# Optimization experiments

Hardware: AMD Instinct MI355X
Metric: run time of the kernel (lower is better)

## Reference

```python
import jax, jax.numpy as jnp
import numpy as np

B, S, G, F, L = 8192, 1152, 576, 16, 24  # batch, n_sites, n_symm, features, lattice side
NP = 576  # number of plaquette correlators (= L^2)


def log_cosh(t):
    # numerically stable log(cosh(t)) as in netket.nn.log_cosh
    a = jnp.abs(t)
    return a + jnp.log1p(jnp.exp(-2.0 * a)) - jnp.log(2.0)


def setup_inputs() -> dict:
    key = jax.random.key(0)
    k = jax.random.split(key, 22)
    p = lambda kk, shape: 0.01 * jax.random.normal(kk, shape, jnp.float32)
    inp = {
        "x": jax.random.normal(k[0], (B, S), jnp.float32),
        "hidden_bias": p(k[1], (F,)),
        "symm_kernel": p(k[2], (F, S)),
        "visible_bias": p(k[3], (2,)),
        "corr0_bias": p(k[4], (1,)),
        "corr0_kernel": p(k[5], (F, NP)),
        "corr1_bias": p(k[6], (1,)),
        "corr1_kernel": p(k[7], (F, L)),
        "corr2_bias": p(k[8], (1,)),
        "corr2_kernel": p(k[9], (F, L)),
        "loop0_hidden_bias": p(k[10], (F,)),
        "loop0_kernel": p(k[11], (F, L)),
        "loop1_hidden_bias": p(k[12], (F,)),
        "loop1_kernel": p(k[13], (F, L)),
        "symmetries": jax.random.randint(k[14], (G, S), 0, S, jnp.int32),
        "corr0_idx": jax.random.randint(k[15], (NP, 4), 0, S, jnp.int32),
        "corr0_symm": jax.random.randint(k[16], (G, NP), 0, NP, jnp.int32),
        "corr1_idx": jax.random.randint(k[17], (L, L), 0, S, jnp.int32),
        "corr1_symm": jax.random.randint(k[18], (G, L), 0, L, jnp.int32),
        "corr2_idx": jax.random.randint(k[19], (L, L), 0, S, jnp.int32),
        "corr2_symm": jax.random.randint(k[20], (G, L), 0, L, jnp.int32),
    }
    return inp


def reference(x, hidden_bias, symm_kernel, visible_bias,
              corr0_bias, corr0_kernel, corr1_bias, corr1_kernel,
              corr2_bias, corr2_kernel,
              loop0_hidden_bias, loop0_kernel, loop1_hidden_bias, loop1_kernel,
              symmetries, corr0_idx, corr0_symm, corr1_idx, corr1_symm,
              corr2_idx, corr2_symm):
    # symmetrized single-spin term: (B, F, G)
    theta = jnp.einsum('bs,fgs->bfg', x, symm_kernel[:, symmetries])
    theta = theta + hidden_bias[None, :, None]
    # sublattice visible bias: (B,)
    bias = jnp.sum(x.reshape(x.shape[0], -1, 2), axis=1) @ visible_bias

    corr_vals = []
    for idx, sidx, cb, ck in ((corr0_idx, corr0_symm, corr0_bias, corr0_kernel),
                              (corr1_idx, corr1_symm, corr1_bias, corr1_kernel),
                              (corr2_idx, corr2_symm, corr2_bias, corr2_kernel)):
        cv = jnp.take(x, idx, axis=1).prod(axis=2)  # (B, n_corr)
        corr_vals.append(cv)
        theta = theta + jnp.einsum('bc,fgc->bfg', cv, ck[:, sidx])
        bias = bias + cb[0] * jnp.sum(cv, axis=1)

    out = jnp.sum(log_cosh(theta), axis=(1, 2)) + bias

    # extra hidden units for the last two (loop) correlators
    for cv, sidx, lhb, lk in ((corr_vals[1], corr1_symm, loop0_hidden_bias, loop0_kernel),
                              (corr_vals[2], corr2_symm, loop1_hidden_bias, loop1_kernel)):
        lt = jnp.einsum('bc,fgc->bfg', cv, lk[:, sidx]) + lhb[None, :, None]
        out = out + jnp.sum(log_cosh(lt), axis=(1, 2))
    return out
```

## Files before the change

### kernel.cpp

```cpp
#include <hip/hip_runtime.h>
#include <hip/hip_bf16.h>

#define B_   8192
#define S_   1152
#define G_   576
#define F_   16
#define L_   24
#define NP_  576
#define KA   1856
#define NCOL 9216
#define KV   1984

typedef float f32x4 __attribute__((ext_vector_type(4)));
typedef short short8_t __attribute__((ext_vector_type(8)));

__device__ __forceinline__ short f2bf(float v) {
  unsigned u = __float_as_uint(v);
  unsigned r = (u + 0x7fffu + ((u >> 16) & 1u)) >> 16;
  return (short)r;
}
__device__ __forceinline__ float bf2f(short s) {
  return __uint_as_float(((unsigned)(unsigned short)s) << 16);
}

__device__ __forceinline__ float log_cosh_f(float t) {
  float a = fabsf(t);
  return a + __logf(1.f + __expf(-2.f * a)) - 0.6931471805599453f;
}

__device__ __forceinline__ float wave_sum(float v) {
  #pragma unroll
  for (int d = 1; d < 64; d <<= 1) v += __shfl_xor(v, d, 64);
  return v;
}

__device__ __forceinline__ void load_lds16(const void* g, void* l) {
  __builtin_amdgcn_global_load_lds(
      (const __attribute__((address_space(1))) void*)g,
      (__attribute__((address_space(3))) void*)l, 16, 0, 0);
}

__global__ __launch_bounds__(256) void build_a_kernel(
    const float* __restrict__ x, const float* __restrict__ vb,
    const float* __restrict__ cb0, const float* __restrict__ cb1,
    const float* __restrict__ cb2,
    const int* __restrict__ idx0, const int* __restrict__ idx1,
    const int* __restrict__ idx2,
    short* __restrict__ A, float* __restrict__ out) {
  int b = blockIdx.x, t = threadIdx.x;
  __shared__ float xs[S_];
  __shared__ float red[20];
  float se = 0.f, so = 0.f, s0 = 0.f, s1 = 0.f, s2 = 0.f;
  const float* xr = x + (size_t)b * S_;
  short* Ar = A + (size_t)b * KA;

  for (int i = t; i < S_; i += 256) {
    float v = xr[i];
    xs[i] = v;
    Ar[i] = f2bf(v);
    if (i & 1) so += v; else se += v;
  }
  __syncthreads();

  for (int c = t; c < NP_; c += 256) {
    const int* q = idx0 + c * 4;
    float p = xs[q[0]] * xs[q[1]] * xs[q[2]] * xs[q[3]];
    s0 += p;
    Ar[S_ + c] = f2bf(p);
  }
  if (t < L_) {
    const int* q = idx1 + t * L_;
    float p = 1.f;
    #pragma unroll
    for (int j = 0; j < L_; ++j) p *= xs[q[j]];
    s1 = p;
    short hi = f2bf(p);
    Ar[1728 + t] = hi;
    Ar[1752 + t] = f2bf(p - bf2f(hi));
  }
  if (t >= 32 && t < 32 + L_) {
    int l = t - 32;
    const int* q = idx2 + l * L_;
    float p = 1.f;
    #pragma unroll
    for (int j = 0; j < L_; ++j) p *= xs[q[j]];
    s2 = p;
    short hi = f2bf(p);
    Ar[1792 + l] = hi;
    Ar[1816 + l] = f2bf(p - bf2f(hi));
  }
  if (t >= 64 && t < 80) Ar[1776 + (t - 64)] = 0;
  if (t >= 80 && t < 96) Ar[1840 + (t - 80)] = 0;

  se = wave_sum(se); so = wave_sum(so);
  s0 = wave_sum(s0); s1 = wave_sum(s1); s2 = wave_sum(s2);
  int w = t >> 6;
  if ((t & 63) == 0) {
    red[w] = se; red[4 + w] = so; red[8 + w] = s0;
    red[12 + w] = s1; red[16 + w] = s2;
  }
  __syncthreads();
  if (t == 0) {
    float a  = red[0] + red[1] + red[2] + red[3];
    float bb = red[4] + red[5] + red[6] + red[7];
    float c0 = red[8] + red[9] + red[10] + red[11];
    float c1 = red[12] + red[13] + red[14] + red[15];
    float c2 = red[16] + red[17] + red[18] + red[19];
    out[b] = vb[0] * a + vb[1] * bb + cb0[0] * c0 + cb1[0] * c1 + cb2[0] * c2;
  }
}

__global__ __launch_bounds__(256) void build_w_kernel(
    const float* __restrict__ symm_kernel, const int* __restrict__ symmetries,
    const float* __restrict__ c0k, const int* __restrict__ c0s,
    const float* __restrict__ c1k, const int* __restrict__ c1s,
    const float* __restrict__ c2k, const int* __restrict__ c2s,
    const float* __restrict__ l0k, const float* __restrict__ l1k,
    short* __restrict__ Wt, short* __restrict__ Wlt) {
  const int CHUNKS = KV / 8;
  int t = blockIdx.x * 256 + threadIdx.x;
  int n = t / CHUNKS;
  if (n >= NCOL) return;
  int ch = t - n * CHUNKS;
  int g = n >> 4, f = n & 15;
  int k0 = ch * 8;
  short8_t pack;
  #pragma unroll
  for (int j = 0; j < 8; ++j) {
    int k = k0 + j;
    float val;
    if (k < 1152) {
      val = symm_kernel[f * S_ + symmetries[g * S_ + k]];
    } else if (k < 1728) {
      int c = k - 1152;
      val = c0k[f * NP_ + c0s[g * NP_ + c]];
    } else if (k < 1792) {
      int c = k - 1728;
      val = (c < 48) ? c1k[f * L_ + c1s[g * L_ + (c < 24 ? c : c - 24)]] : 0.f;
    } else if (k < 1856) {
      int c = k - 1792;
      val = (c < 48) ? c2k[f * L_ + c2s[g * L_ + (c < 24 ? c : c - 24)]] : 0.f;
    } else if (k < 1920) {
      int c = k - 1856;
      val = (c < 48) ? l0k[f * L_ + c1s[g * L_ + (c < 24 ? c : c - 24)]] : 0.f;
    } else {
      int c = k - 1920;
      val = (c < 48) ? l1k[f * L_ + c2s[g * L_ + (c < 24 ? c : c - 24)]] : 0.f;
    }
    pack[j] = f2bf(val);
  }
  if (k0 < KA) *(short8_t*)(Wt + (size_t)n * KA + k0) = pack;
  else         *(short8_t*)(Wlt + (size_t)n * 128 + (k0 - KA)) = pack;
}

__global__ __launch_bounds__(256) void gemm_fused(
    const short* __restrict__ A, const short* __restrict__ Wt,
    const short* __restrict__ Wlt,
    const float* __restrict__ hidden_bias, const float* __restrict__ l0hb,
    const float* __restrict__ l1hb, float* __restrict__ out) {
  __shared__ short Als[3][128 * 64];
  __shared__ short Bls[3][128 * 64];
  const int tid = threadIdx.x;
  const int w = tid >> 6, lane = tid & 63;
  const int wm = w >> 1, wn = w & 1;
  const int lr = lane & 15, lg = lane >> 4;

  const int bid = blockIdx.x;
  const int xcd = bid & 7;
  const int idx = bid >> 3;
  const int st  = idx >> 6;
  const int u   = idx & 63;
  const int m0 = (xcd * 8 + (u & 7)) * 128;
  const int n0 = (st * 8 + (u >> 3)) * 128;

  const int srow = tid >> 3;
  const int scol = ((tid & 7) ^ (srow & 7)) * 16;

  f32x4 acc[4][4];
  float rs[4][4];
  #pragma unroll
  for (int i = 0; i < 4; ++i)
    #pragma unroll
    for (int j = 0; j < 4; ++j) {
      #pragma unroll
      for (int q = 0; q < 4; ++q) acc[i][j][q] = 0.f;
      rs[i][j] = 0.f;
    }

  const char* Abase = (const char*)A + (size_t)m0 * (KA * 2);
  const char* Wbase = (const char*)Wt + (size_t)n0 * (KA * 2);
  const char* Lbase = (const char*)Wlt + (size_t)n0 * 256;

  auto stage = [&](int buf, size_t aOff, const char* bSrc, size_t bStride, size_t bOff) {
    #pragma unroll
    for (int i = 0; i < 4; ++i) {
      int row = i * 32 + srow;
      load_lds16(Abase + (size_t)row * (KA * 2) + aOff + scol,
                 (char*)&Als[buf][0] + (i * 256 + w * 64) * 16);
      load_lds16(bSrc + (size_t)row * bStride + bOff + scol,
                 (char*)&Bls[buf][0] + (i * 256 + w * 64) * 16);
    }
  };

  auto compute = [&](int buf) {
    #pragma unroll
    for (int kk = 0; kk < 2; ++kk) {
      short8_t af[4], wf[4];
      #pragma unroll
      for (int mi = 0; mi < 4; ++mi) {
        int row = wm * 64 + mi * 16 + lr;
        af[mi] = *(const short8_t*)&Als[buf][row * 64 + (((kk * 4 + lg) ^ (lr & 7)) * 8)];
      }
      #pragma unroll
      for (int ni = 0; ni < 4; ++ni) {
        int row = wn * 64 + ni * 16 + lr;
        wf[ni] = *(const short8_t*)&Bls[buf][row * 64 + (((kk * 4 + lg) ^ (lr & 7)) * 8)];
      }
      #pragma unroll
      for (int mi = 0; mi < 4; ++mi)
        #pragma unroll
        for (int ni = 0; ni < 4; ++ni)
          acc[mi][ni] = __builtin_amdgcn_mfma_f32_16x16x32_bf16(af[mi], wf[ni], acc[mi][ni], 0, 0, 0);
    }
  };

  const size_t WS = (size_t)(KA * 2);

  stage(0, 0, Wbase, WS, 0);
  stage(1, 128, Wbase, WS, 128);

  int bc = 0;
  for (int t = 0; t < 29; ++t) {
    if (t + 2 <= 28) {
      int bs = bc + 2; if (bs >= 3) bs -= 3;
      stage(bs, (size_t)(t + 2) * 128, Wbase, WS, (size_t)(t + 2) * 128);
    }
    __builtin_amdgcn_sched_barrier(0);
    if (t < 27)       asm volatile("s_waitcnt vmcnt(16)" ::: "memory");
    else if (t == 27) asm volatile("s_waitcnt vmcnt(8)" ::: "memory");
    else              asm volatile("s_waitcnt vmcnt(0)" ::: "memory");
    __builtin_amdgcn_sched_barrier(0);
    __builtin_amdgcn_s_barrier();
    __builtin_amdgcn_sched_barrier(0);
    compute(bc);
    __builtin_amdgcn_sched_barrier(0);
    __builtin_amdgcn_s_barrier();
    __builtin_amdgcn_sched_barrier(0);
    bc = bc + 1; if (bc >= 3) bc = 0;
  }

  stage(0, (size_t)1728 * 2, Lbase, 256, 0);
  stage(1, (size_t)1792 * 2, Lbase, 256, 128);

  {
    float hb = hidden_bias[lr];
    #pragma unroll
    for (int mi = 0; mi < 4; ++mi)
      #pragma unroll
      for (int i = 0; i < 4; ++i) {
        float s = 0.f;
        #pragma unroll
        for (int ni = 0; ni < 4; ++ni) s += log_cosh_f(acc[mi][ni][i] + hb);
        rs[mi][i] += s;
      }
  }
  __syncthreads();

  #pragma unroll
  for (int pass = 0; pass < 2; ++pass) {
    #pragma unroll
    for (int i = 0; i < 4; ++i)
      #pragma unroll
      for (int j = 0; j < 4; ++j)
        #pragma unroll
        for (int q = 0; q < 4; ++q) acc[i][j][q] = 0.f;

    compute(pass);

    float lb = (pass == 0 ? l0hb : l1hb)[lr];
    #pragma unroll
    for (int mi = 0; mi < 4; ++mi)
      #pragma unroll
      for (int i = 0; i < 4; ++i) {
        float s = 0.f;
        #pragma unroll
        for (int ni = 0; ni < 4; ++ni) s += log_cosh_f(acc[mi][ni][i] + lb);
        rs[mi][i] += s;
      }
  }

  #pragma unroll
  for (int mi = 0; mi < 4; ++mi)
    #pragma unroll
    for (int i = 0; i < 4; ++i) {
      float v = rs[mi][i];
      v += __shfl_xor(v, 1, 64);
      v += __shfl_xor(v, 2, 64);
      v += __shfl_xor(v, 4, 64);
      v += __shfl_xor(v, 8, 64);
      if (lr == 0) atomicAdd(&out[m0 + wm * 64 + mi * 16 + lg * 4 + i], v);
    }
}

extern "C" void kernel_launch(void* const* d_in, const int* in_sizes, int n_in,
                              void* d_out, int out_size, void* d_ws, size_t ws_size,
                              hipStream_t stream) {
  const float* x            = (const float*)d_in[0];
  const float* hidden_bias  = (const float*)d_in[1];
  const float* symm_kernel  = (const float*)d_in[2];
  const float* visible_bias = (const float*)d_in[3];
  const float* corr0_bias   = (const float*)d_in[4];
  const float* corr0_kernel = (const float*)d_in[5];
  const float* corr1_bias   = (const float*)d_in[6];
  const float* corr1_kernel = (const float*)d_in[7];
  const float* corr2_bias   = (const float*)d_in[8];
  const float* corr2_kernel = (const float*)d_in[9];
  const float* l0hb         = (const float*)d_in[10];
  const float* l0k          = (const float*)d_in[11];
  const float* l1hb         = (const float*)d_in[12];
  const float* l1k          = (const float*)d_in[13];
  const int* symmetries     = (const int*)d_in[14];
  const int* idx0           = (const int*)d_in[15];
  const int* c0s            = (const int*)d_in[16];
  const int* idx1           = (const int*)d_in[17];
  const int* c1s            = (const int*)d_in[18];
  const int* idx2           = (const int*)d_in[19];
  const int* c2s            = (const int*)d_in[20];

  short* A   = (short*)d_ws;
  short* Wt  = (short*)((char*)d_ws + 30408704);
  short* Wlt = (short*)((char*)d_ws + 64618496);
  float* out = (float*)d_out;

  build_a_kernel<<<B_, 256, 0, stream>>>(x, visible_bias, corr0_bias, corr1_bias,
                                         corr2_bias, idx0, idx1, idx2, A, out);
  build_w_kernel<<<(NCOL * (KV / 8)) / 256, 256, 0, stream>>>(
      symm_kernel, symmetries, corr0_kernel, c0s, corr1_kernel, c1s,
      corr2_kernel, c2s, l0k, l1k, Wt, Wlt);
  gemm_fused<<<4608, 256, 0, stream>>>(
      A, Wt, Wlt, hidden_bias, l0hb, l1hb, out);
}
```

Baseline: 893.8 us.

## Enlarge GEMM tiles to 256x256 with 512 threads and double buffering

The fused GEMM block tile grows from 128x128 to 256x256 with 8 waves, each computing a 128x64 sub-tile. The LDS pipeline goes from triple to double buffering, and global pointers are advanced incrementally instead of recomputed. The grid is remapped to 32x36 tiles per XCD group. The aim is more reuse of each staged tile and less global/L2 traffic per FLOP. In exchange, each thread holds more accumulator registers, occupancy drops, and there is less prefetch depth to hide latency.

Result: slower. 1.022 ms (+14.3%).

```diff
diff --git a/kernel.cpp b/kernel.cpp
--- a/kernel.cpp
+++ b/kernel.cpp
@@ -153,109 +153,119 @@
   else         *(short8_t*)(Wlt + (size_t)n * 128 + (k0 - KA)) = pack;
 }
 
-__global__ __launch_bounds__(256) void gemm_fused(
+__global__ __launch_bounds__(512) void gemm_fused(
     const short* __restrict__ A, const short* __restrict__ Wt,
     const short* __restrict__ Wlt,
     const float* __restrict__ hidden_bias, const float* __restrict__ l0hb,
     const float* __restrict__ l1hb, float* __restrict__ out) {
-  __shared__ short Als[3][128 * 64];
-  __shared__ short Bls[3][128 * 64];
+  __shared__ short Als[2][256 * 64];
+  __shared__ short Bls[2][256 * 64];
   const int tid = threadIdx.x;
   const int w = tid >> 6, lane = tid & 63;
-  const int wm = w >> 1, wn = w & 1;
+  const int wm = w >> 2, wn = w & 3;
   const int lr = lane & 15, lg = lane >> 4;
 
   const int bid = blockIdx.x;
   const int xcd = bid & 7;
-  const int idx = bid >> 3;
-  const int st  = idx >> 6;
-  const int u   = idx & 63;
-  const int m0 = (xcd * 8 + (u & 7)) * 128;
-  const int n0 = (st * 8 + (u >> 3)) * 128;
+  const int j   = bid >> 3;
+  const int mt  = (xcd << 2) | (j & 3);
+  const int nt  = j >> 2;
+  const int m0 = mt * 256, n0 = nt * 256;
 
   const int srow = tid >> 3;
   const int scol = ((tid & 7) ^ (srow & 7)) * 16;
 
-  f32x4 acc[4][4];
-  float rs[4][4];
-  #pragma unroll
-  for (int i = 0; i < 4; ++i)
-    #pragma unroll
-    for (int j = 0; j < 4; ++j) {
-      #pragma unroll
-      for (int q = 0; q < 4; ++q) acc[i][j][q] = 0.f;
-      rs[i][j] = 0.f;
+  f32x4 acc[8][4];
+  float rs[8][4];
+  #pragma unroll
+  for (int i = 0; i < 8; ++i)
+    #pragma unroll
+    for (int jj = 0; jj < 4; ++jj) {
+      #pragma unroll
+      for (int q = 0; q < 4; ++q) acc[i][jj][q] = 0.f;
+      rs[i][jj] = 0.f;
     }
 
   const char* Abase = (const char*)A + (size_t)m0 * (KA * 2);
   const char* Wbase = (const char*)Wt + (size_t)n0 * (KA * 2);
   const char* Lbase = (const char*)Wlt + (size_t)n0 * 256;
 
-  auto stage = [&](int buf, size_t aOff, const char* bSrc, size_t bStride, size_t bOff) {
+  const char* pA[4];
+  const char* pB[4];
+  #pragma unroll
+  for (int i = 0; i < 4; ++i) {
+    pA[i] = Abase + (size_t)(i * 64 + srow) * (KA * 2) + scol;
+    pB[i] = Wbase + (size_t)(i * 64 + srow) * (KA * 2) + scol;
+  }
+
+  auto stage_main = [&](int buf) {
     #pragma unroll
     for (int i = 0; i < 4; ++i) {
-      int row = i * 32 + srow;
+      load_lds16(pA[i], (char*)&Als[buf][0] + (i * 512 + tid) * 16);
+      load_lds16(pB[i], (char*)&Bls[buf][0] + (i * 512 + tid) * 16);
+      pA[i] += 128;
+      pB[i] += 128;
+    }
+  };
+
+  auto stage_pass = [&](int buf, size_t aOff, size_t bOff) {
+    #pragma unroll
+    for (int i = 0; i < 4; ++i) {
+      int row = i * 64 + srow;
       load_lds16(Abase + (size_t)row * (KA * 2) + aOff + scol,
-                 (char*)&Als[buf][0] + (i * 256 + w * 64) * 16);
-      load_lds16(bSrc + (size_t)row * bStride + bOff + scol,
-                 (char*)&Bls[buf][0] + (i * 256 + w * 64) * 16);
+                 (char*)&Als[buf][0] + (i * 512 + tid) * 16);
+      load_lds16(Lbase + (size_t)row * 256 + bOff + scol,
+                 (char*)&Bls[buf][0] + (i * 512 + tid) * 16);
     }
   };
 
   auto compute = [&](int buf) {
     #pragma unroll
     for (int kk = 0; kk < 2; ++kk) {
-      short8_t af[4], wf[4];
-      #pragma unroll
-      for (int mi = 0; mi < 4; ++mi) {
-        int row = wm * 64 + mi * 16 + lr;
-        af[mi] = *(const short8_t*)&Als[buf][row * 64 + (((kk * 4 + lg) ^ (lr & 7)) * 8)];
+      short8_t af[8], wf[4];
+      #pragma unroll
+      for (int mi = 0; mi < 8; ++mi) {
+        int r = wm * 128 + mi * 16 + lr;
+        af[mi] = *(const short8_t*)&Als[buf][r * 64 + (((kk * 4 + lg) ^ (lr & 7)) * 8)];
       }
       #pragma unroll
       for (int ni = 0; ni < 4; ++ni) {
-        int row = wn * 64 + ni * 16 + lr;
-        wf[ni] = *(const short8_t*)&Bls[buf][row * 64 + (((kk * 4 + lg) ^ (lr & 7)) * 8)];
+        int r = wn * 64 + ni * 16 + lr;
+        wf[ni] = *(const short8_t*)&Bls[buf][r * 64 + (((kk * 4 + lg) ^ (lr & 7)) * 8)];
       }
       #pragma unroll
-      for (int mi = 0; mi < 4; ++mi)
+      for (int mi = 0; mi < 8; ++mi)
         #pragma unroll
         for (int ni = 0; ni < 4; ++ni)
           acc[mi][ni] = __builtin_amdgcn_mfma_f32_16x16x32_bf16(af[mi], wf[ni], acc[mi][ni], 0, 0, 0);
     }
   };
 
-  const size_t WS = (size_t)(KA * 2);
-
-  stage(0, 0, Wbase, WS, 0);
-  stage(1, 128, Wbase, WS, 128);
-
-  int bc = 0;
+  stage_main(0);
+
+  int cur = 0;
   for (int t = 0; t < 29; ++t) {
-    if (t + 2 <= 28) {
-      int bs = bc + 2; if (bs >= 3) bs -= 3;
-      stage(bs, (size_t)(t + 2) * 128, Wbase, WS, (size_t)(t + 2) * 128);
-    }
-    __builtin_amdgcn_sched_barrier(0);
-    if (t < 27)       asm volatile("s_waitcnt vmcnt(16)" ::: "memory");
-    else if (t == 27) asm volatile("s_waitcnt vmcnt(8)" ::: "memory");
-    else              asm volatile("s_waitcnt vmcnt(0)" ::: "memory");
+    if (t < 28) stage_main(cur ^ 1);
+    __builtin_amdgcn_sched_barrier(0);
+    if (t < 28) asm volatile("s_waitcnt vmcnt(8)" ::: "memory");
+    else        asm volatile("s_waitcnt vmcnt(0)" ::: "memory");
     __builtin_amdgcn_sched_barrier(0);
     __builtin_amdgcn_s_barrier();
     __builtin_amdgcn_sched_barrier(0);
-    compute(bc);
+    compute(cur);
     __builtin_amdgcn_sched_barrier(0);
     __builtin_amdgcn_s_barrier();
     __builtin_amdgcn_sched_barrier(0);
-    bc = bc + 1; if (bc >= 3) bc = 0;
-  }
-
-  stage(0, (size_t)1728 * 2, Lbase, 256, 0);
-  stage(1, (size_t)1792 * 2, Lbase, 256, 128);
+    cur ^= 1;
+  }
+
+  stage_pass(0, (size_t)1728 * 2, 0);
+  stage_pass(1, (size_t)1792 * 2, 128);
 
   {
     float hb = hidden_bias[lr];
     #pragma unroll
-    for (int mi = 0; mi < 4; ++mi)
+    for (int mi = 0; mi < 8; ++mi)
       #pragma unroll
       for (int i = 0; i < 4; ++i) {
         float s = 0.f;
@@ -269,17 +279,17 @@
   #pragma unroll
   for (int pass = 0; pass < 2; ++pass) {
     #pragma unroll
-    for (int i = 0; i < 4; ++i)
-      #pragma unroll
-      for (int j = 0; j < 4; ++j)
+    for (int i = 0; i < 8; ++i)
+      #pragma unroll
+      for (int jj = 0; jj < 4; ++jj)
         #pragma unroll
-        for (int q = 0; q < 4; ++q) acc[i][j][q] = 0.f;
+        for (int q = 0; q < 4; ++q) acc[i][jj][q] = 0.f;
 
     compute(pass);
 
     float lb = (pass == 0 ? l0hb : l1hb)[lr];
     #pragma unroll
-    for (int mi = 0; mi < 4; ++mi)
+    for (int mi = 0; mi < 8; ++mi)
       #pragma unroll
       for (int i = 0; i < 4; ++i) {
         float s = 0.f;
@@ -290,7 +300,7 @@
   }
 
   #pragma unroll
-  for (int mi = 0; mi < 4; ++mi)
+  for (int mi = 0; mi < 8; ++mi)
     #pragma unroll
     for (int i = 0; i < 4; ++i) {
       float v = rs[mi][i];
@@ -298,7 +308,7 @@
       v += __shfl_xor(v, 2, 64);
       v += __shfl_xor(v, 4, 64);
       v += __shfl_xor(v, 8, 64);
-      if (lr == 0) atomicAdd(&out[m0 + wm * 64 + mi * 16 + lg * 4 + i], v);
+      if (lr == 0) atomicAdd(&out[m0 + wm * 128 + mi * 16 + lg * 4 + i], v);
     }
 }
 
@@ -337,6 +347,6 @@
   build_w_kernel<<<(NCOL * (KV / 8)) / 256, 256, 0, stream>>>(
       symm_kernel, symmetries, corr0_kernel, c0s, corr1_kernel, c1s,
       corr2_kernel, c2s, l0k, l1k, Wt, Wlt);
-  gemm_fused<<<4608, 256, 0, stream>>>(
+  gemm_fused<<<(B_ / 256) * (NCOL / 256), 512, 0, stream>>>(
       A, Wt, Wlt, hidden_bias, l0hb, l1hb, out);
 }
```

## Widen GEMM tile to 128x256 and precompute staging pointers

Applied to the files above, without the earlier changes.

The fused GEMM now has each block compute a 128x256 output tile instead of 128x128. Each wave holds 4x8 MFMA accumulators, and the B staging buffer doubles, so each A tile loaded from memory is reused across twice as many columns and the grid is halved. Global-to-LDS load addresses are now precomputed per thread and advanced incrementally, and the vmcnt waits are adjusted for the extra loads in flight. The costs are higher register pressure (128 accumulator floats), more LDS per block, and likely lower occupancy.

After: 821.1 us. 1.09x faster.

```diff
diff --git a/kernel.cpp b/kernel.cpp
--- a/kernel.cpp
+++ b/kernel.cpp
@@ -153,13 +153,14 @@
   else         *(short8_t*)(Wlt + (size_t)n * 128 + (k0 - KA)) = pack;
 }
 
-__global__ __launch_bounds__(256) void gemm_fused(
+__global__ __launch_bounds__(256)
+void gemm_fused(
     const short* __restrict__ A, const short* __restrict__ Wt,
     const short* __restrict__ Wlt,
     const float* __restrict__ hidden_bias, const float* __restrict__ l0hb,
     const float* __restrict__ l1hb, float* __restrict__ out) {
   __shared__ short Als[3][128 * 64];
-  __shared__ short Bls[3][128 * 64];
+  __shared__ short Bls[3][256 * 64];
   const int tid = threadIdx.x;
   const int w = tid >> 6, lane = tid & 63;
   const int wm = w >> 1, wn = w & 1;
@@ -167,77 +168,99 @@
 
   const int bid = blockIdx.x;
   const int xcd = bid & 7;
-  const int idx = bid >> 3;
-  const int st  = idx >> 6;
-  const int u   = idx & 63;
-  const int m0 = (xcd * 8 + (u & 7)) * 128;
-  const int n0 = (st * 8 + (u >> 3)) * 128;
+  const int j   = bid >> 3;
+  const int mt  = (xcd << 3) | (j & 7);
+  const int nt  = j >> 3;
+  const int m0 = mt * 128, n0 = nt * 256;
 
   const int srow = tid >> 3;
   const int scol = ((tid & 7) ^ (srow & 7)) * 16;
 
-  f32x4 acc[4][4];
-  float rs[4][4];
+  f32x4 acc[4][8];
   #pragma unroll
   for (int i = 0; i < 4; ++i)
     #pragma unroll
-    for (int j = 0; j < 4; ++j) {
-      #pragma unroll
-      for (int q = 0; q < 4; ++q) acc[i][j][q] = 0.f;
-      rs[i][j] = 0.f;
-    }
+    for (int jj = 0; jj < 8; ++jj)
+      #pragma unroll
+      for (int q = 0; q < 4; ++q) acc[i][jj][q] = 0.f;
 
   const char* Abase = (const char*)A + (size_t)m0 * (KA * 2);
   const char* Wbase = (const char*)Wt + (size_t)n0 * (KA * 2);
   const char* Lbase = (const char*)Wlt + (size_t)n0 * 256;
 
-  auto stage = [&](int buf, size_t aOff, const char* bSrc, size_t bStride, size_t bOff) {
+  const char* pA[4];
+  const char* pB[8];
+  #pragma unroll
+  for (int i = 0; i < 4; ++i)
+    pA[i] = Abase + (size_t)(i * 32 + srow) * (KA * 2) + scol;
+  #pragma unroll
+  for (int i = 0; i < 8; ++i)
+    pB[i] = Wbase + (size_t)(i * 32 + srow) * (KA * 2) + scol;
+
+  auto stage_main = [&](int buf) {
+    #pragma unroll
+    for (int i = 0; i < 4; ++i) {
+      load_lds16(pA[i], (char*)&Als[buf][0] + (i * 256 + tid) * 16);
+      pA[i] += 128;
+    }
+    #pragma unroll
+    for (int i = 0; i < 8; ++i) {
+      load_lds16(pB[i], (char*)&Bls[buf][0] + (i * 256 + tid) * 16);
+      pB[i] += 128;
+    }
+  };
+
+  auto stage_pass = [&](int buf, size_t aOff, size_t bOff) {
     #pragma unroll
     for (int i = 0; i < 4; ++i) {
       int row = i * 32 + srow;
       load_lds16(Abase + (size_t)row * (KA * 2) + aOff + scol,
-                 (char*)&Als[buf][0] + (i * 256 + w * 64) * 16);
-      load_lds16(bSrc + (size_t)row * bStride + bOff + scol,
-                 (char*)&Bls[buf][0] + (i * 256 + w * 64) * 16);
+                 (char*)&Als[buf][0] + (i * 256 + tid) * 16);
+    }
+    #pragma unroll
+    for (int i = 0; i < 8; ++i) {
+      int row = i * 32 + srow;
+      load_lds16(Lbase + (size_t)row * 256 + bOff + scol,
+                 (char*)&Bls[buf][0] + (i * 256 + tid) * 16);
     }
   };
 
   auto compute = [&](int buf) {
     #pragma unroll
     for (int kk = 0; kk < 2; ++kk) {
-      short8_t af[4], wf[4];
+      const int co = (((kk * 4 + lg) ^ (lr & 7)) * 8);
+      short8_t af[4], wf[8];
       #pragma unroll
       for (int mi = 0; mi < 4; ++mi) {
-        int row = wm * 64 + mi * 16 + lr;
-        af[mi] = *(const short8_t*)&Als[buf][row * 64 + (((kk * 4 + lg) ^ (lr & 7)) * 8)];
+        int r = wm * 64 + mi * 16 + lr;
+        af[mi] = *(const short8_t*)&Als[buf][r * 64 + co];
       }
       #pragma unroll
-      for (int ni = 0; ni < 4; ++ni) {
-        int row = wn * 64 + ni * 16 + lr;
-        wf[ni] = *(const short8_t*)&Bls[buf][row * 64 + (((kk * 4 + lg) ^ (lr & 7)) * 8)];
+      for (int ni = 0; ni < 8; ++ni) {
+        int r = wn * 128 + ni * 16 + lr;
+        wf[ni] = *(const short8_t*)&Bls[buf][r * 64 + co];
       }
       #pragma unroll
       for (int mi = 0; mi < 4; ++mi)
         #pragma unroll
-        for (int ni = 0; ni < 4; ++ni)
-          acc[mi][ni] = __builtin_amdgcn_mfma_f32_16x16x32_bf16(af[mi], wf[ni], acc[mi][ni], 0, 0, 0);
+        for (int ni = 0; ni < 8; ++ni)
+          acc[mi][ni] = __builtin_amdgcn_mfma_f32_16x16x32_bf16(
+              af[mi], wf[ni], acc[mi][ni], 0, 0, 0);
     }
   };
 
-  const size_t WS = (size_t)(KA * 2);
-
-  stage(0, 0, Wbase, WS, 0);
-  stage(1, 128, Wbase, WS, 128);
+  stage_main(0);
+  stage_main(1);
 
   int bc = 0;
   for (int t = 0; t < 29; ++t) {
     if (t + 2 <= 28) {
       int bs = bc + 2; if (bs >= 3) bs -= 3;
-      stage(bs, (size_t)(t + 2) * 128, Wbase, WS, (size_t)(t + 2) * 128);
-    }
-    __builtin_amdgcn_sched_barrier(0);
-    if (t < 27)       asm volatile("s_waitcnt vmcnt(16)" ::: "memory");
-    else if (t == 27) asm volatile("s_waitcnt vmcnt(8)" ::: "memory");
+      stage_main(bs);
+    }
+    __builtin_amdgcn_sched_barrier(0);
+    if (t < 27)       asm volatile("s_waitcnt vmcnt(24)" ::: "memory");
+    else if (t == 27) asm volatile("s_waitcnt vmcnt(12)" ::: "memory");
     else              asm volatile("s_waitcnt vmcnt(0)" ::: "memory");
     __builtin_amdgcn_sched_barrier(0);
     __builtin_amdgcn_s_barrier();
@@ -249,19 +272,19 @@
     bc = bc + 1; if (bc >= 3) bc = 0;
   }
 
-  stage(0, (size_t)1728 * 2, Lbase, 256, 0);
-  stage(1, (size_t)1792 * 2, Lbase, 256, 128);
-
+  stage_pass(0, (size_t)1728 * 2, 0);
+  stage_pass(1, (size_t)1792 * 2, 128);
+
+  float rs[4][4];
   {
-    float hb = hidden_bias[lr];
     #pragma unroll
     for (int mi = 0; mi < 4; ++mi)
       #pragma unroll
       for (int i = 0; i < 4; ++i) {
         float s = 0.f;
         #pragma unroll
-        for (int ni = 0; ni < 4; ++ni) s += log_cosh_f(acc[mi][ni][i] + hb);
-        rs[mi][i] += s;
+        for (int ni = 0; ni < 8; ++ni) s += log_cosh_f(acc[mi][ni][i] + hidden_bias[lr]);
+        rs[mi][i] = s;
       }
   }
   __syncthreads();
@@ -271,20 +294,20 @@
     #pragma unroll
     for (int i = 0; i < 4; ++i)
       #pragma unroll
-      for (int j = 0; j < 4; ++j)
+      for (int jj = 0; jj < 8; ++jj)
         #pragma unroll
-        for (int q = 0; q < 4; ++q) acc[i][j][q] = 0.f;
+        for (int q = 0; q < 4; ++q) acc[i][jj][q] = 0.f;
 
     compute(pass);
 
-    float lb = (pass == 0 ? l0hb : l1hb)[lr];
+    const float* lb = (pass == 0 ? l0hb : l1hb);
     #pragma unroll
     for (int mi = 0; mi < 4; ++mi)
       #pragma unroll
       for (int i = 0; i < 4; ++i) {
         float s = 0.f;
         #pragma unroll
-        for (int ni = 0; ni < 4; ++ni) s += log_cosh_f(acc[mi][ni][i] + lb);
+        for (int ni = 0; ni < 8; ++ni) s += log_cosh_f(acc[mi][ni][i] + lb[lr]);
         rs[mi][i] += s;
       }
   }
@@ -337,6 +360,6 @@
   build_w_kernel<<<(NCOL * (KV / 8)) / 256, 256, 0, stream>>>(
       symm_kernel, symmetries, corr0_kernel, c0s, corr1_kernel, c1s,
       corr2_kernel, c2s, l0k, l1k, Wt, Wlt);
-  gemm_fused<<<4608, 256, 0, stream>>>(
+  gemm_fused<<<(B_ / 128) * (NCOL / 256), 256, 0, stream>>>(
       A, Wt, Wlt, hidden_bias, l0hb, l1hb, out);
 }
```
